# Kernel tuning notes

Measured on AMD Instinct MI355X. Metric: run time of the kernel, lower is better.

The kernel has to match this reference:

```python
import jax, jax.numpy as jnp
import numpy as np

DIM = 512
NUM_HEADS = 8
HEAD_DIM = DIM // NUM_HEADS
SCALE = HEAD_DIM ** -0.5


def setup_inputs() -> dict:
    key = jax.random.key(0)
    kx, kqw, kqb, kpw, kpb = jax.random.split(key, 5)
    B, N = 2, 4096
    x = jax.random.normal(kx, (B, N, DIM), dtype=jnp.float32)
    # nn.Linear weights stored as [out, in]; init ~ U(-1/sqrt(in), 1/sqrt(in))
    bound = 1.0 / np.sqrt(DIM)
    qkv_w = jax.random.uniform(kqw, (3 * DIM, DIM), minval=-bound, maxval=bound, dtype=jnp.float32)
    qkv_b = jax.random.uniform(kqb, (3 * DIM,), minval=-bound, maxval=bound, dtype=jnp.float32)
    proj_w = jax.random.uniform(kpw, (DIM, DIM), minval=-bound, maxval=bound, dtype=jnp.float32)
    proj_b = jax.random.uniform(kpb, (DIM,), minval=-bound, maxval=bound, dtype=jnp.float32)
    return {"x": x, "qkv_w": qkv_w, "qkv_b": qkv_b, "proj_w": proj_w, "proj_b": proj_b}


def reference(x, qkv_w, qkv_b, proj_w, proj_b):
    B, N, C = x.shape
    # qkv: [B, N, 3C] -> [3, B, H, N, Dh]
    qkv = x @ qkv_w.T + qkv_b
    qkv = qkv.reshape(B, N, 3, NUM_HEADS, HEAD_DIM).transpose(2, 0, 3, 1, 4)
    q, k, v = qkv[0], qkv[1], qkv[2]
    # scores: [B, H, N, N] (materialized, matching the original math)
    attn = jnp.einsum("bhqd,bhkd->bhqk", q, k) * SCALE
    attn = jax.nn.softmax(attn, axis=-1)
    out = jnp.einsum("bhqk,bhkd->bhqd", attn, v)  # [B, H, N, Dh]
    out = out.transpose(0, 2, 1, 3).reshape(B, N, C)
    return out @ proj_w.T + proj_b
```

## Files before the change

### kernel.cpp

```cpp
#include <hip/hip_runtime.h>
#include <hip/hip_bf16.h>
#include <stdint.h>
#include <stddef.h>

typedef __attribute__((ext_vector_type(8))) short short8;
typedef __attribute__((ext_vector_type(4))) float f32x4;
typedef __attribute__((ext_vector_type(16))) float f32x16;

#define MFMA16(a, b, c) __builtin_amdgcn_mfma_f32_16x16x32_bf16((a), (b), (c), 0, 0, 0)
#define MFMA32(a, b, c) __builtin_amdgcn_mfma_f32_32x32x16_bf16((a), (b), (c), 0, 0, 0)

#define QSCALE 0.1803368801111204f

#if __has_builtin(__builtin_amdgcn_exp2f)
#define EXP2(x) __builtin_amdgcn_exp2f(x)
#else
#define EXP2(x) __builtin_exp2f(x)
#endif

__device__ __forceinline__ float b2f(short x) {
    unsigned u = ((unsigned)(unsigned short)x) << 16;
    float f; __builtin_memcpy(&f, &u, 4); return f;
}
__device__ __forceinline__ short f2b(float f) {
    unsigned u; __builtin_memcpy(&u, &f, 4);
    u = (u + 0x7FFFu + ((u >> 16) & 1u)) >> 16;
    return (short)u;
}
__device__ __forceinline__ unsigned pack2(float a, float b) {
    unsigned ua, ub; __builtin_memcpy(&ua, &a, 4); __builtin_memcpy(&ub, &b, 4);
    return __builtin_amdgcn_perm(ub + 0x8000u, ua + 0x8000u, 0x07060302u);
}
__device__ __forceinline__ short8 load8f(const float* p) {
    const float4 f0 = *(const float4*)p;
    const float4 f1 = *(const float4*)(p + 4);
    short8 r;
    r[0]=f2b(f0.x); r[1]=f2b(f0.y); r[2]=f2b(f0.z); r[3]=f2b(f0.w);
    r[4]=f2b(f1.x); r[5]=f2b(f1.y); r[6]=f2b(f1.z); r[7]=f2b(f1.w);
    return r;
}

__global__ __launch_bounds__(256) void cvt3(
    const float* __restrict__ s0, short* __restrict__ d0, int n0,
    const float* __restrict__ s1, short* __restrict__ d1, int n1,
    const float* __restrict__ s2, short* __restrict__ d2, int n2)
{
    int i = blockIdx.x * 256 + threadIdx.x;
    if (i < n0) { *(short8*)(d0 + (size_t)i * 8) = load8f(s0 + (size_t)i * 8); return; }
    i -= n0;
    if (i < n1) { *(short8*)(d1 + (size_t)i * 8) = load8f(s1 + (size_t)i * 8); return; }
    i -= n1;
    if (i < n2) { *(short8*)(d2 + (size_t)i * 8) = load8f(s2 + (size_t)i * 8); }
}

__global__ __launch_bounds__(256) void qkv_gemm(
    const short* __restrict__ X, const short* __restrict__ W,
    const float* __restrict__ bias,
    short* __restrict__ Qb, short* __restrict__ Kb, short* __restrict__ Vb)
{
    __shared__ short sT[128][132];

    const int tid  = threadIdx.x;
    const int wv   = tid >> 6;
    const int lane = tid & 63;
    const int l15  = lane & 15;
    const int quad = lane >> 4;
    const int m0   = blockIdx.x * 128 + (wv >> 1) * 64;
    const int sec  = blockIdx.y >> 2;
    const int bis  = blockIdx.y & 3;
    const int nbase = sec * 512 + bis * 128;
    const int j0   = (wv & 1) * 64;

    const f32x4 zero = {0.f, 0.f, 0.f, 0.f};
    f32x4 acc[4][4];
#pragma unroll
    for (int i = 0; i < 4; i++)
#pragma unroll
        for (int j = 0; j < 4; j++) acc[i][j] = zero;

    for (int k0 = 0; k0 < 512; k0 += 32) {
        short8 a[4], b[4];
#pragma unroll
        for (int i = 0; i < 4; i++)
            a[i] = *(const short8*)(X + (size_t)(m0 + i * 16 + l15) * 512 + k0 + quad * 8);
#pragma unroll
        for (int j = 0; j < 4; j++)
            b[j] = *(const short8*)(W + (size_t)(nbase + j0 + j * 16 + l15) * 512 + k0 + quad * 8);
#pragma unroll
        for (int i = 0; i < 4; i++)
#pragma unroll
            for (int j = 0; j < 4; j++)
                acc[i][j] = MFMA16(a[i], b[j], acc[i][j]);
    }

    if (sec < 2) {
        const float scale = (sec == 0) ? QSCALE : 1.0f;
        short* dst = (sec == 0) ? Qb : Kb;
#pragma unroll
        for (int j = 0; j < 4; j++) {
            const int jc = bis * 128 + j0 + j * 16 + l15;
            const float bs = bias[sec * 512 + jc];
            const int hl = jc >> 6, d = jc & 63;
#pragma unroll
            for (int i = 0; i < 4; i++) {
#pragma unroll
                for (int r = 0; r < 4; r++) {
                    const int m = m0 + i * 16 + quad * 4 + r;
                    const int bb = m >> 12, seq = m & 4095;
                    dst[((size_t)(bb * 8 + hl) * 4096 + seq) * 64 + d] =
                        f2b((acc[i][j][r] + bs) * scale);
                }
            }
        }
    } else {
#pragma unroll
        for (int j = 0; j < 4; j++) {
            const int jcl = j0 + j * 16 + l15;
            const float bs = bias[nbase + jcl];
#pragma unroll
            for (int i = 0; i < 4; i++) {
                uint2 w;
                w.x = pack2(acc[i][j][0] + bs, acc[i][j][1] + bs);
                w.y = pack2(acc[i][j][2] + bs, acc[i][j][3] + bs);
                *(uint2*)&sT[jcl][(wv >> 1) * 64 + i * 16 + quad * 4] = w;
            }
        }
        __syncthreads();

        const int jcl = tid >> 1, half = tid & 1;
        const int hl = (bis * 128 + jcl) >> 6;
        const int d  = jcl & 63;
        const int bb = (blockIdx.x * 128) >> 12;
        const int seq0 = ((blockIdx.x * 128) & 4095) + half * 64;
        short* dst = Vb + ((size_t)(bb * 8 + hl) * 64 + d) * 4096 + seq0;
#pragma unroll
        for (int u = 0; u < 8; u++)
            *(short8*)(dst + u * 8) = *(const short8*)&sT[jcl][half * 64 + u * 8];
    }
}

__global__ __launch_bounds__(512) void flash_attn(
    const short* __restrict__ Q, const short* __restrict__ K,
    const short* __restrict__ V, short* __restrict__ PO0,
    short* __restrict__ PO1, float* __restrict__ lbuf, int ktiles)
{
    __shared__ short sK[64][72];
    __shared__ short sV[64][72];
    __shared__ short sP[8][32][72];

    const int tid  = threadIdx.x;
    const int wv   = tid >> 6;
    const int lane = tid & 63;
    const int l31  = lane & 31;
    const int half = lane >> 5;
    const int bh = blockIdx.y;
    const int b = bh >> 3, h = bh & 7;
    const int qw = blockIdx.x * 256 + wv * 32;
    const int ks = blockIdx.z;
    const int key0 = ks * ktiles * 64;

    const short* Qb = Q + (size_t)bh * 4096 * 64;
    const short* Kb = K + (size_t)bh * 4096 * 64;
    const short* Vb = V + (size_t)bh * 64 * 4096;

    short8 aq[4];
#pragma unroll
    for (int s = 0; s < 4; s++)
        aq[s] = *(const short8*)(Qb + (size_t)(qw + l31) * 64 + s * 16 + half * 8);

    f32x16 o0 = {}, o1 = {};
    float lsum = 0.f;

    const int srow = tid >> 3, scb = (tid & 7) * 8;
    short8 pk, pv;
    pk = *(const short8*)(Kb + (size_t)(key0 + srow) * 64 + scb);
    pv = *(const short8*)(Vb + (size_t)srow * 4096 + key0 + scb);

    for (int kt = 0; kt < ktiles; ++kt) {
        const int k0 = key0 + kt * 64;
        __syncthreads();
        *(short8*)&sK[srow][scb] = pk;
        *(short8*)&sV[srow][scb] = pv;
        __syncthreads();

        if (kt + 1 < ktiles) {
            const int k0n = k0 + 64;
            pk = *(const short8*)(Kb + (size_t)(k0n + srow) * 64 + scb);
            pv = *(const short8*)(Vb + (size_t)srow * 4096 + k0n + scb);
        }

#pragma unroll
        for (int c = 0; c < 2; c++) {
            f32x16 ST = {};
#pragma unroll
            for (int s = 0; s < 4; s++) {
                const short8 bk = *(const short8*)&sK[c * 32 + l31][s * 16 + half * 8];
                ST = MFMA32(bk, aq[s], ST);
            }
#pragma unroll
            for (int q = 0; q < 4; q++) {
                const float p0 = EXP2(ST[4 * q + 0]), p1 = EXP2(ST[4 * q + 1]);
                const float p2 = EXP2(ST[4 * q + 2]), p3 = EXP2(ST[4 * q + 3]);
                lsum += (p0 + p1) + (p2 + p3);
                uint2 w; w.x = pack2(p0, p1); w.y = pack2(p2, p3);
                *(uint2*)&sP[wv][l31][c * 32 + q * 8 + half * 4] = w;
            }
        }
        __threadfence_block();

        short8 bp[4];
#pragma unroll
        for (int s = 0; s < 4; s++)
            bp[s] = *(const short8*)&sP[wv][l31][s * 16 + half * 8];

#pragma unroll
        for (int s = 0; s < 4; s++) {
            const short8 bv0 = *(const short8*)&sV[l31][s * 16 + half * 8];
            const short8 bv1 = *(const short8*)&sV[32 + l31][s * 16 + half * 8];
            o0 = MFMA32(bv0, bp[s], o0);
            o1 = MFMA32(bv1, bp[s], o1);
        }
        __threadfence_block();
    }

    lsum += __shfl_xor(lsum, 32);
    const float inv = 1.f / fmaxf(lsum, 1e-30f);

    short* PO = (ks == 0) ? PO0 : PO1;
#pragma unroll
    for (int q = 0; q < 4; q++) {
        uint2 w0, w1;
        w0.x = pack2(o0[4 * q + 0] * inv, o0[4 * q + 1] * inv);
        w0.y = pack2(o0[4 * q + 2] * inv, o0[4 * q + 3] * inv);
        w1.x = pack2(o1[4 * q + 0] * inv, o1[4 * q + 1] * inv);
        w1.y = pack2(o1[4 * q + 2] * inv, o1[4 * q + 3] * inv);
        const size_t rowoff = ((size_t)b * 4096 + qw + l31) * 512;
        const int col = h * 64 + q * 8 + half * 4;
        *(uint2*)(PO + rowoff + col) = w0;
        *(uint2*)(PO + rowoff + col + 32) = w1;
    }
    if (half == 0)
        lbuf[((size_t)ks * 16 + bh) * 4096 + qw + l31] = lsum;
}

__global__ __launch_bounds__(256) void combine(
    const short* __restrict__ PO0, const short* __restrict__ PO1,
    short* __restrict__ attn, const float* __restrict__ L)
{
    const int i = blockIdx.x * 256 + threadIdx.x;
    const size_t flat = (size_t)i * 8;
    const int col = (int)(flat & 511);
    const int q   = (int)((flat >> 9) & 4095);
    const int b   = (int)(flat >> 21);
    const int bh  = b * 8 + (col >> 6);
    const float l0 = L[(size_t)bh * 4096 + q];
    const float l1 = L[(size_t)65536 + (size_t)bh * 4096 + q];
    const float inv = 1.f / (l0 + l1);
    const float w0 = l0 * inv, w1 = l1 * inv;
    const short8 a = *(const short8*)(PO0 + flat);
    const short8 c = *(const short8*)(PO1 + flat);
    short8 r;
#pragma unroll
    for (int k = 0; k < 8; k += 2) {
        const unsigned p = pack2(w0 * b2f(a[k]) + w1 * b2f(c[k]),
                                 w0 * b2f(a[k + 1]) + w1 * b2f(c[k + 1]));
        r[k]     = (short)(p & 0xFFFF);
        r[k + 1] = (short)(p >> 16);
    }
    *(short8*)(attn + flat) = r;
}

__global__ __launch_bounds__(256) void proj_gemm(
    const short* __restrict__ A, const short* __restrict__ W,
    const float* __restrict__ bias, float* __restrict__ dst)
{
    const int tid  = threadIdx.x;
    const int wv   = tid >> 6;
    const int lane = tid & 63;
    const int l15  = lane & 15;
    const int quad = lane >> 4;
    const int m0 = blockIdx.x * 128 + (wv >> 1) * 64;
    const int n0 = blockIdx.y * 128 + (wv & 1) * 64;

    const f32x4 zero = {0.f, 0.f, 0.f, 0.f};
    f32x4 acc[4][4];
#pragma unroll
    for (int i = 0; i < 4; i++)
#pragma unroll
        for (int j = 0; j < 4; j++) acc[i][j] = zero;

    for (int k0 = 0; k0 < 512; k0 += 32) {
        short8 a[4], b[4];
#pragma unroll
        for (int i = 0; i < 4; i++)
            a[i] = *(const short8*)(A + (size_t)(m0 + i * 16 + l15) * 512 + k0 + quad * 8);
#pragma unroll
        for (int j = 0; j < 4; j++)
            b[j] = *(const short8*)(W + (size_t)(n0 + j * 16 + l15) * 512 + k0 + quad * 8);
#pragma unroll
        for (int i = 0; i < 4; i++)
#pragma unroll
            for (int j = 0; j < 4; j++)
                acc[i][j] = MFMA16(a[i], b[j], acc[i][j]);
    }

#pragma unroll
    for (int j = 0; j < 4; j++) {
        const int n = n0 + j * 16 + l15;
        const float bs = bias[n];
#pragma unroll
        for (int i = 0; i < 4; i++) {
#pragma unroll
            for (int r = 0; r < 4; r++) {
                const int m = m0 + i * 16 + quad * 4 + r;
                dst[(size_t)m * 512 + n] = acc[i][j][r] + bs;
            }
        }
    }
}

extern "C" void kernel_launch(void* const* d_in, const int* in_sizes, int n_in,
                              void* d_out, int out_size, void* d_ws, size_t ws_size,
                              hipStream_t stream)
{
    const float* x      = (const float*)d_in[0];
    const float* qkv_w  = (const float*)d_in[1];
    const float* qkv_b  = (const float*)d_in[2];
    const float* proj_w = (const float*)d_in[3];
    const float* proj_b = (const float*)d_in[4];

    const size_t MB = 1024 * 1024;
    short* xb   = (short*)d_out;
    short* wb   = (short*)d_out + 4 * MB;
    short* PO0  = (short*)d_out;
    short* PO1  = (short*)d_out + 4 * MB;
    float* out  = (float*)d_out;

    short* Qf = (short*)d_ws;
    short* Kf = Qf + (size_t)16 * 4096 * 64;
    short* Vf = Kf + (size_t)16 * 4096 * 64;
    short* attn = Qf;
    float* lbuf = (float*)((char*)d_ws + 24 * MB);
    short* pwb  = (short*)((char*)d_ws + 24 * MB + 512 * 1024);

    cvt3<<<2560, 256, 0, stream>>>(x, xb, 524288, qkv_w, wb, 98304, proj_w, pwb, 32768);
    qkv_gemm<<<dim3(64, 12), 256, 0, stream>>>(xb, wb, qkv_b, Qf, Kf, Vf);
    flash_attn<<<dim3(16, 16, 2), 512, 0, stream>>>(Qf, Kf, Vf, PO0, PO1, lbuf, 32);
    combine<<<2048, 256, 0, stream>>>(PO0, PO1, attn, lbuf);
    proj_gemm<<<dim3(64, 4), 256, 0, stream>>>(attn, pwb, proj_b, out);
}
```

Baseline: 251.0 us.

## Keep attention probabilities in registers and double key tile per iteration

The flash attention kernel no longer writes the exponentiated scores to shared memory and reads them back. The 32x32 MFMA output layout is fed directly as the B operand of the PV MFMA, with the V tile's columns permuted in shared memory when it is stored so the key ordering matches. The key tile grows from 64 to 128 per iteration, halving the number of barrier pairs, and launch bounds now request 4 waves per SIMD. The risks are higher register pressure and a subtle layout permutation that must be exactly right for correctness.

```diff
diff --git a/kernel.cpp b/kernel.cpp
--- a/kernel.cpp
+++ b/kernel.cpp
@@ -139,14 +139,13 @@
     }
 }
 
-__global__ __launch_bounds__(512) void flash_attn(
+__global__ __launch_bounds__(512, 4) void flash_attn(
     const short* __restrict__ Q, const short* __restrict__ K,
     const short* __restrict__ V, short* __restrict__ PO0,
-    short* __restrict__ PO1, float* __restrict__ lbuf, int ktiles)
-{
-    __shared__ short sK[64][72];
-    __shared__ short sV[64][72];
-    __shared__ short sP[8][32][72];
+    short* __restrict__ PO1, float* __restrict__ lbuf, int niter)
+{
+    __shared__ short sK[128][72];
+    __shared__ short sV[64][136];
 
     const int tid  = threadIdx.x;
     const int wv   = tid >> 6;
@@ -157,7 +156,7 @@
     const int b = bh >> 3, h = bh & 7;
     const int qw = blockIdx.x * 256 + wv * 32;
     const int ks = blockIdx.z;
-    const int key0 = ks * ktiles * 64;
+    const int key0 = ks * niter * 128;
 
     const short* Qb = Q + (size_t)bh * 4096 * 64;
     const short* Kb = K + (size_t)bh * 4096 * 64;
@@ -171,56 +170,64 @@
     f32x16 o0 = {}, o1 = {};
     float lsum = 0.f;
 
-    const int srow = tid >> 3, scb = (tid & 7) * 8;
-    short8 pk, pv;
-    pk = *(const short8*)(Kb + (size_t)(key0 + srow) * 64 + scb);
-    pv = *(const short8*)(Vb + (size_t)srow * 4096 + key0 + scb);
-
-    for (int kt = 0; kt < ktiles; ++kt) {
-        const int k0 = key0 + kt * 64;
+    const int r0  = tid >> 3;
+    const int scb = (tid & 7) * 8;
+    const int vb  = (scb & ~12) | ((scb & 8) >> 1);
+
+    short8 pk0, pk1, pv0, pv1;
+    pk0 = *(const short8*)(Kb + (size_t)(key0 + r0) * 64 + scb);
+    pk1 = *(const short8*)(Kb + (size_t)(key0 + 64 + r0) * 64 + scb);
+    pv0 = *(const short8*)(Vb + (size_t)r0 * 4096 + key0 + scb);
+    pv1 = *(const short8*)(Vb + (size_t)r0 * 4096 + key0 + 64 + scb);
+
+    for (int kt = 0; kt < niter; ++kt) {
         __syncthreads();
-        *(short8*)&sK[srow][scb] = pk;
-        *(short8*)&sV[srow][scb] = pv;
+        *(short8*)&sK[r0][scb]      = pk0;
+        *(short8*)&sK[64 + r0][scb] = pk1;
+        *(uint2*)&sV[r0][vb]          = ((const uint2*)&pv0)[0];
+        *(uint2*)&sV[r0][vb + 8]      = ((const uint2*)&pv0)[1];
+        *(uint2*)&sV[r0][64 + vb]     = ((const uint2*)&pv1)[0];
+        *(uint2*)&sV[r0][64 + vb + 8] = ((const uint2*)&pv1)[1];
         __syncthreads();
 
-        if (kt + 1 < ktiles) {
-            const int k0n = k0 + 64;
-            pk = *(const short8*)(Kb + (size_t)(k0n + srow) * 64 + scb);
-            pv = *(const short8*)(Vb + (size_t)srow * 4096 + k0n + scb);
-        }
-
-#pragma unroll
-        for (int c = 0; c < 2; c++) {
+        if (kt + 1 < niter) {
+            const int kn = key0 + (kt + 1) * 128;
+            pk0 = *(const short8*)(Kb + (size_t)(kn + r0) * 64 + scb);
+            pk1 = *(const short8*)(Kb + (size_t)(kn + 64 + r0) * 64 + scb);
+            pv0 = *(const short8*)(Vb + (size_t)r0 * 4096 + kn + scb);
+            pv1 = *(const short8*)(Vb + (size_t)r0 * 4096 + kn + 64 + scb);
+        }
+
+#pragma unroll
+        for (int c = 0; c < 4; c++) {
             f32x16 ST = {};
 #pragma unroll
             for (int s = 0; s < 4; s++) {
                 const short8 bk = *(const short8*)&sK[c * 32 + l31][s * 16 + half * 8];
                 ST = MFMA32(bk, aq[s], ST);
             }
-#pragma unroll
-            for (int q = 0; q < 4; q++) {
-                const float p0 = EXP2(ST[4 * q + 0]), p1 = EXP2(ST[4 * q + 1]);
-                const float p2 = EXP2(ST[4 * q + 2]), p3 = EXP2(ST[4 * q + 3]);
-                lsum += (p0 + p1) + (p2 + p3);
-                uint2 w; w.x = pack2(p0, p1); w.y = pack2(p2, p3);
-                *(uint2*)&sP[wv][l31][c * 32 + q * 8 + half * 4] = w;
-            }
-        }
-        __threadfence_block();
-
-        short8 bp[4];
-#pragma unroll
-        for (int s = 0; s < 4; s++)
-            bp[s] = *(const short8*)&sP[wv][l31][s * 16 + half * 8];
-
-#pragma unroll
-        for (int s = 0; s < 4; s++) {
-            const short8 bv0 = *(const short8*)&sV[l31][s * 16 + half * 8];
-            const short8 bv1 = *(const short8*)&sV[32 + l31][s * 16 + half * 8];
-            o0 = MFMA32(bv0, bp[s], o0);
-            o1 = MFMA32(bv1, bp[s], o1);
-        }
-        __threadfence_block();
+            float e[16];
+#pragma unroll
+            for (int r = 0; r < 16; r++) e[r] = EXP2(ST[r]);
+#pragma unroll
+            for (int r = 0; r < 16; r += 4)
+                lsum += (e[r] + e[r + 1]) + (e[r + 2] + e[r + 3]);
+            uint4 w0 = { pack2(e[0], e[1]),  pack2(e[2], e[3]),
+                         pack2(e[4], e[5]),  pack2(e[6], e[7]) };
+            uint4 w1 = { pack2(e[8], e[9]),  pack2(e[10], e[11]),
+                         pack2(e[12], e[13]), pack2(e[14], e[15]) };
+            const short8 bp0 = *(const short8*)&w0;
+            const short8 bp1 = *(const short8*)&w1;
+
+            const short8 bv00 = *(const short8*)&sV[l31][(2 * c) * 16 + half * 8];
+            const short8 bv01 = *(const short8*)&sV[32 + l31][(2 * c) * 16 + half * 8];
+            o0 = MFMA32(bv00, bp0, o0);
+            o1 = MFMA32(bv01, bp0, o1);
+            const short8 bv10 = *(const short8*)&sV[l31][(2 * c + 1) * 16 + half * 8];
+            const short8 bv11 = *(const short8*)&sV[32 + l31][(2 * c + 1) * 16 + half * 8];
+            o0 = MFMA32(bv10, bp1, o0);
+            o1 = MFMA32(bv11, bp1, o1);
+        }
     }
 
     lsum += __shfl_xor(lsum, 32);
@@ -345,7 +352,7 @@
 
     cvt3<<<2560, 256, 0, stream>>>(x, xb, 524288, qkv_w, wb, 98304, proj_w, pwb, 32768);
     qkv_gemm<<<dim3(64, 12), 256, 0, stream>>>(xb, wb, qkv_b, Qf, Kf, Vf);
-    flash_attn<<<dim3(16, 16, 2), 512, 0, stream>>>(Qf, Kf, Vf, PO0, PO1, lbuf, 32);
+    flash_attn<<<dim3(16, 16, 2), 512, 0, stream>>>(Qf, Kf, Vf, PO0, PO1, lbuf, 16);
     combine<<<2048, 256, 0, stream>>>(PO0, PO1, attn, lbuf);
     proj_gemm<<<dim3(64, 4), 256, 0, stream>>>(attn, pwb, proj_b, out);
 }
```

New measurement: 243.2 us. 1.03x faster.
